# Optimization experiments

Measured on AMD Instinct MI355X. Metric: run time of the kernel, lower is better.

The kernel has to match this reference:

```python
import jax, jax.numpy as jnp
import numpy as np

N_SRC = 1_000_000
N_OUT = 65_536
D = 64

def setup_inputs() -> dict:
    key = jax.random.key(0)
    k1, k2, k3 = jax.random.split(key, 3)
    input = jax.random.normal(k1, (N_OUT, D), dtype=jnp.float32)
    index = jax.random.randint(k2, (N_SRC, D), 0, N_OUT, dtype=jnp.int64)
    src = jax.random.normal(k3, (N_SRC, D), dtype=jnp.float32)
    return {"input": input, "index": index, "src": src}

def reference(input, index, src):
    # torch.scatter_reduce(input, 0, index, src, reduce='sum', include_self=True):
    #   out = input.copy(); out[index[i, j], j] += src[i, j]
    cols = jnp.arange(src.shape[1])[None, :]  # [1, D] broadcasts against index [N, D]
    return input.at[index, cols].add(src)
```

## Files before the change

### kernel.cpp

```cpp
#include <hip/hip_runtime.h>


typedef unsigned int u32;
typedef unsigned short u16;
typedef unsigned long long u64;

#define NBKT 256
#define NBLK 1024
#define BLK  512
#define BATCH 2048
#define CAPR 320
#define CAPS 24
#define TILE 16384
#define OMAX 130048

__global__ void Zero_kernel(u32* p, int n) {
    int i = threadIdx.x;
    if (i < n) p[i] = 0;
}

__global__ void InitOut_kernel(const float4* __restrict__ in, float4* __restrict__ out, int n4) {
    int i = blockIdx.x * blockDim.x + threadIdx.x;
    if (i < n4) out[i] = in[i];
}

__global__ void FallbackAdd_kernel(const int4* __restrict__ index4,
                                   const float4* __restrict__ src4,
                                   float* __restrict__ out, int n4) {
    const int stride = gridDim.x * blockDim.x;
    for (int i = blockIdx.x * blockDim.x + threadIdx.x; i < n4; i += stride) {
        int4 idx = index4[i];
        float4 v = src4[i];
        int jbase = (i & 15) << 2;
        atomicAdd(&out[(idx.x << 6) + jbase + 0], v.x);
        atomicAdd(&out[(idx.y << 6) + jbase + 1], v.y);
        atomicAdd(&out[(idx.z << 6) + jbase + 2], v.z);
        atomicAdd(&out[(idx.w << 6) + jbase + 3], v.w);
    }
}

__global__ __launch_bounds__(BLK) void Scatter_kernel(
        const int* __restrict__ index, const float* __restrict__ src,
        float* __restrict__ val, u16* __restrict__ dst, u16* __restrict__ cntg,
        u32* __restrict__ ocnt, u64* __restrict__ olist,
        int epb, long long E)
{
    __shared__ float sv[NBKT][CAPS];
    __shared__ u16  sd[NBKT][CAPS];
    __shared__ u32  cnt[NBKT];
    __shared__ u32  flushed[NBKT];
    const int t = threadIdx.x;
    const int k = blockIdx.x;
    long long c0 = (long long)k * epb;
    long long c1 = c0 + epb; if (c1 > E) c1 = E;
    if (c0 >= c1) {
        if (t < NBKT) cntg[(size_t)k * NBKT + t] = 0;
        return;
    }
    if (t < NBKT) { cnt[t] = 0; flushed[t] = 0; }
    __syncthreads();

    const int col0 = (t << 2) & 63;
    const size_t rbase = (size_t)k * CAPR;

#define PROC(rr, vv, cc) { \
    int bb = (rr) >> 8; \
    u32 p = atomicAdd(&cnt[bb], 1u); \
    if (p < CAPR) { \
        u32 fl = flushed[bb]; \
        u32 slot = p - fl; \
        u16 dd = (u16)((((rr) & 255) << 6) | (cc)); \
        if (slot < CAPS) { sv[bb][slot] = (vv); sd[bb][slot] = dd; } \
        else { size_t pos = (size_t)bb * (NBLK * CAPR) + rbase + p; \
               val[pos] = (vv); dst[pos] = dd; } \
    } else { \
        u32 oi = atomicAdd(ocnt, 1u); \
        if (oi < OMAX) \
            olist[oi] = ((u64)__float_as_uint(vv) << 32) | (u32)(((rr) << 6) + (cc)); \
    } }

    long long e = c0 + t * 4;
    int4 r; float4 v;
    bool have = e < c1;
    if (have) { r = *(const int4*)(index + e); v = *(const float4*)(src + e); }

    const int g = t >> 3, lr = t & 7;

    for (long long eb = c0; eb < c1; eb += BATCH) {
        if (have) {
            PROC(r.x, v.x, col0 + 0);
            PROC(r.y, v.y, col0 + 1);
            PROC(r.z, v.z, col0 + 2);
            PROC(r.w, v.w, col0 + 3);
        }
        long long en = e + BATCH;
        bool haveN = en < c1;
        int4 rn; float4 vn;
        if (haveN) { rn = *(const int4*)(index + en); vn = *(const float4*)(src + en); }
        __syncthreads();
        #pragma unroll
        for (int pass = 0; pass < 4; ++pass) {
            int b = (pass << 6) + g;
            u32 c = cnt[b]; if (c > CAPR) c = CAPR;
            u32 fl = flushed[b];
            u32 staged = c - fl;
            u32 fcopy, rem, newfl;
            if (staged > CAPS) { fcopy = CAPS; rem = 0; newfl = c; }
            else { fcopy = staged & ~7u; rem = staged - fcopy; newfl = fl + fcopy; }
            size_t rb = (size_t)b * (NBLK * CAPR) + rbase + fl;
            for (u32 i = lr; i < fcopy; i += 8) {
                val[rb + i] = sv[b][i];
                dst[rb + i] = sd[b][i];
            }
            if (lr < rem) {
                sv[b][lr] = sv[b][fcopy + lr];
                sd[b][lr] = sd[b][fcopy + lr];
            }
            if (lr == 0) flushed[b] = newfl;
        }
        __syncthreads();
        r = rn; v = vn; have = haveN; e = en;
    }

    #pragma unroll
    for (int pass = 0; pass < 4; ++pass) {
        int b = (pass << 6) + g;
        u32 c = cnt[b]; if (c > CAPR) c = CAPR;
        u32 fl = flushed[b];
        u32 staged = c - fl;
        u32 fcopy = staged > CAPS ? CAPS : staged;
        size_t rb = (size_t)b * (NBLK * CAPR) + rbase + fl;
        for (u32 i = lr; i < fcopy; i += 8) {
            val[rb + i] = sv[b][i];
            dst[rb + i] = sd[b][i];
        }
    }
    __syncthreads();
    if (t < NBKT) {
        u32 c = cnt[t]; if (c > CAPR) c = CAPR;
        cntg[(size_t)k * NBKT + t] = (u16)c;
    }
#undef PROC
}

__global__ __launch_bounds__(1024) void Reduce_kernel(
        const float* __restrict__ val, const u16* __restrict__ dst,
        const u16* __restrict__ cntg, const u32* __restrict__ ocnt,
        const u64* __restrict__ olist,
        const float* __restrict__ input, float* __restrict__ out)
{
    __shared__ float tile[TILE];
    const int b = blockIdx.x, t = threadIdx.x;
    float4* t4 = (float4*)tile;
    for (int i = t; i < TILE / 4; i += 1024) t4[i] = make_float4(0.f, 0.f, 0.f, 0.f);
    __syncthreads();
    const int g = t >> 3, lr = t & 7;
    const size_t bb = (size_t)b * (NBLK * CAPR);
    for (int k = g; k < NBLK; k += 128) {
        u32 n = cntg[(size_t)k * NBKT + b]; if (n > CAPR) n = CAPR;
        const float* vp = val + bb + (size_t)k * CAPR;
        const u16*  dp = dst + bb + (size_t)k * CAPR;
        for (u32 i = lr; i < n; i += 8)
            atomicAdd(&tile[dp[i]], vp[i]);
    }
    __syncthreads();
    u32 on = *ocnt; if (on > OMAX) on = OMAX;
    for (u32 i = t; i < on; i += 1024) {
        u64 pr = olist[i];
        u32 d = (u32)pr;
        if ((d >> 14) == (u32)b)
            atomicAdd(&tile[d & (TILE - 1)], __uint_as_float((u32)(pr >> 32)));
    }
    __syncthreads();
    const float4* in4 = (const float4*)(input + (size_t)b * TILE);
    float4* o4 = (float4*)(out + (size_t)b * TILE);
    for (int i = t; i < TILE / 4; i += 1024) {
        float4 a = in4[i], s = t4[i];
        a.x += s.x; a.y += s.y; a.z += s.z; a.w += s.w;
        o4[i] = a;
    }
}

extern "C" void kernel_launch(void* const* d_in, const int* in_sizes, int n_in,
                              void* d_out, int out_size, void* d_ws, size_t ws_size,
                              hipStream_t stream) {
    const float* input = (const float*)d_in[0];
    const int*   index = (const int*)d_in[1];
    const float* src   = (const float*)d_in[2];
    float* out = (float*)d_out;
    long long E = (long long)in_sizes[2];

    const size_t off_olist = 64;
    const size_t off_cnt   = off_olist + (size_t)OMAX * 8;
    const size_t off_val   = (size_t)2u << 20;
    const size_t off_dst   = off_val + (size_t)NBKT * NBLK * CAPR * 4;
    const size_t need      = off_dst + (size_t)NBKT * NBLK * CAPR * 2;

    int epb = (int)(((E + NBLK - 1) / NBLK + 63) & ~63LL);

    int n4o = out_size / 4;
    if (ws_size < need || (E & 3) || out_size != NBKT * TILE || epb > 65536) {
        InitOut_kernel<<<(n4o + 255) / 256, 256, 0, stream>>>(
            (const float4*)input, (float4*)out, n4o);
        FallbackAdd_kernel<<<2048, 256, 0, stream>>>(
            (const int4*)index, (const float4*)src, out, (int)(E / 4));
        return;
    }

    char* ws = (char*)d_ws;
    u32*  ocnt  = (u32*)ws;
    u64*  olist = (u64*)(ws + off_olist);
    u16*  cntg  = (u16*)(ws + off_cnt);
    float* val  = (float*)(ws + off_val);
    u16*  dst   = (u16*)(ws + off_dst);

    Zero_kernel<<<1, 64, 0, stream>>>(ocnt, 16);

    Scatter_kernel<<<NBLK, BLK, 0, stream>>>(index, src, val, dst, cntg,
                                             ocnt, olist, epb, E);
    Reduce_kernel<<<NBKT, 1024, 0, stream>>>(val, dst, cntg, ocnt, olist, input, out);
}
```

Baseline: 698.1 us.

## Split reduce across two blocks per bucket, vectorize loads, enlarge shared staging

Each bucket's reduce now runs on two 512-thread blocks, each handling half of the scatter-block segments. Each block reads its values and destinations as float4/ushort4 and merges its shared-memory tile into the output with global atomics; the output is first seeded with the input by a separate init kernel. The scatter kernel's shared staging grows from 24 to 30 slots with a padded row, and flushes in groups of 16 to write longer contiguous runs. The aim is more parallelism and fewer load instructions in the reduce phase. The cost is an extra full-output init pass, global atomic traffic on the output, and summation order that is no longer deterministic.

Result: faster. 622.6 us (-10.8%).

```diff
diff --git a/kernel.cpp b/kernel.cpp
--- a/kernel.cpp
+++ b/kernel.cpp
@@ -10,7 +10,9 @@
 #define BLK  512
 #define BATCH 2048
 #define CAPR 320
-#define CAPS 24
+#define CAPS 30
+#define CPAD 31
+#define FU   16
 #define TILE 16384
 #define OMAX 130048
 
@@ -45,8 +47,8 @@
         u32* __restrict__ ocnt, u64* __restrict__ olist,
         int epb, long long E)
 {
-    __shared__ float sv[NBKT][CAPS];
-    __shared__ u16  sd[NBKT][CAPS];
+    __shared__ float sv[NBKT][CPAD];
+    __shared__ u16  sd[NBKT][CPAD];
     __shared__ u32  cnt[NBKT];
     __shared__ u32  flushed[NBKT];
     const int t = threadIdx.x;
@@ -106,15 +108,15 @@
             u32 staged = c - fl;
             u32 fcopy, rem, newfl;
             if (staged > CAPS) { fcopy = CAPS; rem = 0; newfl = c; }
-            else { fcopy = staged & ~7u; rem = staged - fcopy; newfl = fl + fcopy; }
+            else { fcopy = staged & ~(FU - 1u); rem = staged - fcopy; newfl = fl + fcopy; }
             size_t rb = (size_t)b * (NBLK * CAPR) + rbase + fl;
             for (u32 i = lr; i < fcopy; i += 8) {
                 val[rb + i] = sv[b][i];
                 dst[rb + i] = sd[b][i];
             }
-            if (lr < rem) {
-                sv[b][lr] = sv[b][fcopy + lr];
-                sd[b][lr] = sd[b][fcopy + lr];
+            for (u32 i = lr; i < rem; i += 8) {
+                sv[b][i] = sv[b][fcopy + i];
+                sd[b][i] = sd[b][fcopy + i];
             }
             if (lr == 0) flushed[b] = newfl;
         }
@@ -143,42 +145,50 @@
 #undef PROC
 }
 
-__global__ __launch_bounds__(1024) void Reduce_kernel(
+__global__ __launch_bounds__(512) void Reduce_kernel(
         const float* __restrict__ val, const u16* __restrict__ dst,
         const u16* __restrict__ cntg, const u32* __restrict__ ocnt,
-        const u64* __restrict__ olist,
-        const float* __restrict__ input, float* __restrict__ out)
+        const u64* __restrict__ olist, float* __restrict__ out)
 {
     __shared__ float tile[TILE];
-    const int b = blockIdx.x, t = threadIdx.x;
+    const int b = blockIdx.x >> 1;
+    const int p = blockIdx.x & 1;
+    const int t = threadIdx.x;
     float4* t4 = (float4*)tile;
-    for (int i = t; i < TILE / 4; i += 1024) t4[i] = make_float4(0.f, 0.f, 0.f, 0.f);
+    for (int i = t; i < TILE / 4; i += 512) t4[i] = make_float4(0.f, 0.f, 0.f, 0.f);
     __syncthreads();
     const int g = t >> 3, lr = t & 7;
-    const size_t bb = (size_t)b * (NBLK * CAPR);
-    for (int k = g; k < NBLK; k += 128) {
+    const size_t bb = (size_t)b * ((size_t)NBLK * CAPR);
+    for (int k = p * (NBLK / 2) + g; k < (p + 1) * (NBLK / 2); k += 64) {
         u32 n = cntg[(size_t)k * NBKT + b]; if (n > CAPR) n = CAPR;
         const float* vp = val + bb + (size_t)k * CAPR;
         const u16*  dp = dst + bb + (size_t)k * CAPR;
-        for (u32 i = lr; i < n; i += 8)
-            atomicAdd(&tile[dp[i]], vp[i]);
-    }
-    __syncthreads();
-    u32 on = *ocnt; if (on > OMAX) on = OMAX;
-    for (u32 i = t; i < on; i += 1024) {
-        u64 pr = olist[i];
-        u32 d = (u32)pr;
-        if ((d >> 14) == (u32)b)
-            atomicAdd(&tile[d & (TILE - 1)], __uint_as_float((u32)(pr >> 32)));
-    }
-    __syncthreads();
-    const float4* in4 = (const float4*)(input + (size_t)b * TILE);
-    float4* o4 = (float4*)(out + (size_t)b * TILE);
-    for (int i = t; i < TILE / 4; i += 1024) {
-        float4 a = in4[i], s = t4[i];
-        a.x += s.x; a.y += s.y; a.z += s.z; a.w += s.w;
-        o4[i] = a;
-    }
+        u32 n4 = n & ~3u;
+        for (u32 i = lr * 4; i + 4 <= n4 + 4 && i < n4; i += 32) {
+            float4 v = *(const float4*)(vp + i);
+            ushort4 d = *(const ushort4*)(dp + i);
+            atomicAdd(&tile[d.x], v.x);
+            atomicAdd(&tile[d.y], v.y);
+            atomicAdd(&tile[d.z], v.z);
+            atomicAdd(&tile[d.w], v.w);
+        }
+        u32 rem = n - n4;
+        if ((u32)lr < rem)
+            atomicAdd(&tile[dp[n4 + lr]], vp[n4 + lr]);
+    }
+    if (p == 0) {
+        u32 on = *ocnt; if (on > OMAX) on = OMAX;
+        for (u32 i = t; i < on; i += 512) {
+            u64 pr = olist[i];
+            u32 d = (u32)pr;
+            if ((d >> 14) == (u32)b)
+                atomicAdd(&tile[d & (TILE - 1)], __uint_as_float((u32)(pr >> 32)));
+        }
+    }
+    __syncthreads();
+    float* ob = out + (size_t)b * TILE;
+    for (int i = t; i < TILE; i += 512)
+        atomicAdd(&ob[i], tile[i]);
 }
 
 extern "C" void kernel_launch(void* const* d_in, const int* in_sizes, int n_in,
@@ -215,8 +225,10 @@
     u16*  dst   = (u16*)(ws + off_dst);
 
     Zero_kernel<<<1, 64, 0, stream>>>(ocnt, 16);
+    InitOut_kernel<<<(n4o + 255) / 256, 256, 0, stream>>>(
+        (const float4*)input, (float4*)out, n4o);
 
     Scatter_kernel<<<NBLK, BLK, 0, stream>>>(index, src, val, dst, cntg,
                                              ocnt, olist, epb, E);
-    Reduce_kernel<<<NBKT, 1024, 0, stream>>>(val, dst, cntg, ocnt, olist, input, out);
-}
+    Reduce_kernel<<<NBKT * 2, 512, 0, stream>>>(val, dst, cntg, ocnt, olist, out);
+}
```
